# Kernel tuning notes

Measured on AMD Instinct MI355X. Metric: run time of the kernel, lower is better.

Reference implementation:

```python
import jax, jax.numpy as jnp
import numpy as np

B, N, F, H, L = 8, 512, 32, 64, 2

def setup_inputs() -> dict:
    key = jax.random.key(0)
    ks = jax.random.split(key, 16)
    s = lambda fan_in: 1.0 / np.sqrt(fan_in)
    return {
        "x": jax.random.normal(ks[0], (B, N, F), dtype=jnp.float32),
        # node encoder: Linear(F, H), stored as [in, out]
        "W_enc": jax.random.uniform(ks[1], (F, H), minval=-s(F), maxval=s(F)),
        "b_enc": jax.random.uniform(ks[2], (H,), minval=-s(F), maxval=s(F)),
        # edge MLP: Linear(2H, H) then Linear(H, 1)
        "W_e1": jax.random.uniform(ks[3], (2 * H, H), minval=-s(2 * H), maxval=s(2 * H)),
        "b_e1": jax.random.uniform(ks[4], (H,), minval=-s(2 * H), maxval=s(2 * H)),
        "W_e2": jax.random.uniform(ks[5], (H,), minval=-s(H), maxval=s(H)),
        "b_e2": jax.random.uniform(ks[6], (), minval=-s(H), maxval=s(H)),
        # per-layer message Linear(H, H)
        "W_msg": jax.random.uniform(ks[7], (L, H, H), minval=-s(H), maxval=s(H)),
        "b_msg": jax.random.uniform(ks[8], (L, H), minval=-s(H), maxval=s(H)),
        # per-layer GRUCell(H, H): gates ordered [r, z, n], stored as [in, 3H]
        "W_ih": jax.random.uniform(ks[9], (L, H, 3 * H), minval=-s(H), maxval=s(H)),
        "b_ih": jax.random.uniform(ks[10], (L, 3 * H), minval=-s(H), maxval=s(H)),
        "W_hh": jax.random.uniform(ks[11], (L, H, 3 * H), minval=-s(H), maxval=s(H)),
        "b_hh": jax.random.uniform(ks[12], (L, 3 * H), minval=-s(H), maxval=s(H)),
        # output Linear(H, 1)
        "W_out": jax.random.uniform(ks[13], (H, 1), minval=-s(H), maxval=s(H)),
        "b_out": jax.random.uniform(ks[14], (1,), minval=-s(H), maxval=s(H)),
    }

def reference(x, W_enc, b_enc, W_e1, b_e1, W_e2, b_e2, W_msg, b_msg,
              W_ih, b_ih, W_hh, b_hh, W_out, b_out):
    # Node encoding (dropout is eval-mode identity)
    h = jax.nn.relu(x @ W_enc + b_enc)  # [B, N, H]

    # Edge MLP on pairwise concat [h_i, h_j]: split W_e1 so we never build the 2H concat
    Wa, Wb = W_e1[:H], W_e1[H:]
    zi = h @ Wa                           # contribution of h_i, [B, N, H]
    zj = h @ Wb                           # contribution of h_j, [B, N, H]
    e = jax.nn.relu(zi[:, :, None, :] + zj[:, None, :, :] + b_e1)  # [B, N, N, H]
    logits = jnp.einsum('bijh,h->bij', e, W_e2) + b_e2             # [B, N, N]

    eye = jnp.eye(logits.shape[-1], dtype=bool)
    logits = jnp.where(eye[None], -jnp.inf, logits)
    adj = jax.nn.softmax(logits, axis=-1)
    adj = jnp.nan_to_num(adj, nan=0.0, posinf=0.0, neginf=0.0)

    for l in range(L):
        m = jnp.einsum('bij,bjh->bih', adj, h)             # message aggregation
        m = jax.nn.relu(m @ W_msg[l] + b_msg[l])
        # GRUCell update (gates [r, z, n])
        gi = m @ W_ih[l] + b_ih[l]
        gh = h @ W_hh[l] + b_hh[l]
        ir, iz, inn = jnp.split(gi, 3, axis=-1)
        hr, hz, hn = jnp.split(gh, 3, axis=-1)
        r = jax.nn.sigmoid(ir + hr)
        z = jax.nn.sigmoid(iz + hz)
        n = jnp.tanh(inn + r * hn)
        h = (1.0 - z) * n + z * h

    graph_emb = jnp.mean(h, axis=1)       # [B, H]
    return graph_emb @ W_out + b_out      # [B, 1]
```

## Files before the change

kernel.cpp:

```cpp
#include <hip/hip_runtime.h>
#include <math.h>

#define BB 8
#define NN 512
#define FF 32
#define HH 64
#define NEG_BIG (-1.0e30f)

__device__ __forceinline__ float lane_bcast(float v, int l) {
    return __int_as_float(__builtin_amdgcn_readlane(__float_as_int(v), l));
}

__global__ __launch_bounds__(256) void encode_kernel(
    const float* __restrict__ x, const float* __restrict__ W_enc,
    const float* __restrict__ b_enc, const float* __restrict__ W_e1,
    const float* __restrict__ b_e1,
    float* __restrict__ h, float* __restrict__ zi, float* __restrict__ zjT)
{
    const int t = threadIdx.x;
    const int hh = t & 63;
    const int qu = __builtin_amdgcn_readfirstlane(t >> 6);
    const int gR = blockIdx.x * 4 + qu;

    const float xv = x[gR * FF + (hh & 31)];
    float acc = b_enc[hh];
#pragma unroll 8
    for (int k = 0; k < FF; ++k)
        acc = fmaf(lane_bcast(xv, k), W_enc[k * HH + hh], acc);
    const float hval = fmaxf(acc, 0.f);
    h[gR * HH + hh] = hval;

    float z1 = b_e1[hh], z2 = 0.f;
#pragma unroll 8
    for (int k = 0; k < HH; ++k) {
        const float hk = lane_bcast(hval, k);
        z1 = fmaf(hk, W_e1[k * HH + hh], z1);
        z2 = fmaf(hk, W_e1[(HH + k) * HH + hh], z2);
    }
    zi[gR * HH + hh] = z1;
    zjT[((size_t)(gR >> 9) * HH + hh) * NN + (gR & (NN - 1))] = z2;
}

template <int MODE>
__global__ __launch_bounds__(512, 4) void adjlayer_kernel(
    const float* __restrict__ zi, const float* __restrict__ zjT,
    const float* __restrict__ We2, const float* __restrict__ be2,
    float* __restrict__ adjw, const float* __restrict__ h_in,
    const float* __restrict__ Wmsg, const float* __restrict__ bmsg,
    const float* __restrict__ Wih, const float* __restrict__ bih,
    const float* __restrict__ Whh, const float* __restrict__ bhh,
    float* __restrict__ h_out, float* __restrict__ partial)
{
    const int b  = blockIdx.x >> 6;
    const int i0 = (blockIdx.x & 63) << 3;
    const int t  = threadIdx.x;
    const int tj = t & 63;
    const int w  = __builtin_amdgcn_readfirstlane(t >> 6);
    const int gR0 = b * NN + i0;
    const int j   = 64 * w + tj;

    __shared__ float smem[6336];
    __shared__ float mml[8][66];
    __shared__ float hol[8][66];
    __shared__ float redm[8][8];
    __shared__ float reds[8][8];
#define RED(p, r, c)        smem[(((p) * 8) + (r)) * 66 + (c)]
#define GP(h2, k2, r, g, c) smem[(((((h2) * 2 + (k2)) * 8 + (r)) * 3 + (g)) * 66) + (c)]

    hol[w][tj] = h_in[(size_t)(gR0 + w) * HH + tj];

    float va[8];
    if (MODE == 0) {
        const float* zib = zi + (size_t)gR0 * HH;
        const float* ztb = zjT + (size_t)b * HH * NN + j;
        const float bias2 = be2[0];
        float acc[8];
#pragma unroll
        for (int r = 0; r < 8; ++r) acc[r] = bias2;

        for (int kc = 0; kc < 8; ++kc) {
            float zt[8];
#pragma unroll
            for (int kk = 0; kk < 8; ++kk)
                zt[kk] = ztb[(size_t)(kc * 8 + kk) * NN];
#pragma unroll
            for (int kk = 0; kk < 8; ++kk) {
                const int k = kc * 8 + kk;
                const float wk = We2[k];
#pragma unroll
                for (int r = 0; r < 8; ++r) {
                    const float zv = zib[r * HH + k];
                    acc[r] = fmaf(fmaxf(zv + zt[kk], 0.f), wk, acc[r]);
                }
            }
        }
#pragma unroll
        for (int r = 0; r < 8; ++r)
            if (j == i0 + r) acc[r] = NEG_BIG;

#pragma unroll
        for (int r = 0; r < 8; ++r) {
            float m = acc[r];
#pragma unroll
            for (int off = 32; off >= 1; off >>= 1) m = fmaxf(m, __shfl_xor(m, off));
            if (tj == 0) redm[w][r] = m;
        }
        __syncthreads();
        float M[8];
#pragma unroll
        for (int r = 0; r < 8; ++r) {
            float m = redm[0][r];
#pragma unroll
            for (int p = 1; p < 8; ++p) m = fmaxf(m, redm[p][r]);
            M[r] = m;
        }
#pragma unroll
        for (int r = 0; r < 8; ++r) {
            const float e = __expf(acc[r] - M[r]);
            va[r] = e;
            float s = e;
#pragma unroll
            for (int off = 32; off >= 1; off >>= 1) s += __shfl_xor(s, off);
            if (tj == 0) reds[w][r] = s;
        }
        __syncthreads();
#pragma unroll
        for (int r = 0; r < 8; ++r) {
            float s = reds[0][r];
#pragma unroll
            for (int p = 1; p < 8; ++p) s += reds[p][r];
            va[r] *= 1.0f / s;
            adjw[(size_t)(gR0 + r) * NN + j] = va[r];
        }
    } else {
#pragma unroll
        for (int r = 0; r < 8; ++r)
            va[r] = adjw[(size_t)(gR0 + r) * NN + j];
    }

    {
        const float* hq = h_in + ((size_t)b * NN + 64 * w) * HH + tj;
        float mac[8] = {0.f, 0.f, 0.f, 0.f, 0.f, 0.f, 0.f, 0.f};
#pragma unroll 4
        for (int jj = 0; jj < 64; ++jj) {
            const float hv = hq[(size_t)jj * HH];
#pragma unroll
            for (int r = 0; r < 8; ++r)
                mac[r] = fmaf(lane_bcast(va[r], jj), hv, mac[r]);
        }
#pragma unroll
        for (int r = 0; r < 8; ++r) RED(w, r, tj) = mac[r];
    }
    __syncthreads();

    {
        float m = RED(0, w, tj);
#pragma unroll
        for (int p = 1; p < 8; ++p) m += RED(p, w, tj);
        float mmv = bmsg[tj];
#pragma unroll 8
        for (int k = 0; k < HH; ++k)
            mmv = fmaf(lane_bcast(m, k), Wmsg[k * HH + tj], mmv);
        mml[w][tj] = fmaxf(mmv, 0.f);
    }
    __syncthreads();

    {
        const int half = w >> 2, kh = (w >> 1) & 1, rq = w & 1;
        const float* Wg = half ? Whh : Wih;
        const float* bg = half ? bhh : bih;
        float sreg[4];
#pragma unroll
        for (int r = 0; r < 4; ++r)
            sreg[r] = half ? hol[rq * 4 + r][tj] : mml[rq * 4 + r][tj];
        float g0[4], g1[4], g2[4];
#pragma unroll
        for (int r = 0; r < 4; ++r) {
            g0[r] = kh ? 0.f : bg[tj];
            g1[r] = kh ? 0.f : bg[64 + tj];
            g2[r] = kh ? 0.f : bg[128 + tj];
        }
        const int k0 = kh * 32;
#pragma unroll 4
        for (int kk = 0; kk < 32; ++kk) {
            const float* wk = Wg + (size_t)(k0 + kk) * 192;
            const float w0 = wk[tj], w1 = wk[64 + tj], w2 = wk[128 + tj];
#pragma unroll
            for (int r = 0; r < 4; ++r) {
                const float s = lane_bcast(sreg[r], k0 + kk);
                g0[r] = fmaf(s, w0, g0[r]);
                g1[r] = fmaf(s, w1, g1[r]);
                g2[r] = fmaf(s, w2, g2[r]);
            }
        }
#pragma unroll
        for (int r = 0; r < 4; ++r) {
            GP(half, kh, rq * 4 + r, 0, tj) = g0[r];
            GP(half, kh, rq * 4 + r, 1, tj) = g1[r];
            GP(half, kh, rq * 4 + r, 2, tj) = g2[r];
        }
    }
    __syncthreads();

    float hnew;
    {
        const float ir  = GP(0, 0, w, 0, tj) + GP(0, 1, w, 0, tj);
        const float iz  = GP(0, 0, w, 1, tj) + GP(0, 1, w, 1, tj);
        const float inn = GP(0, 0, w, 2, tj) + GP(0, 1, w, 2, tj);
        const float hr  = GP(1, 0, w, 0, tj) + GP(1, 1, w, 0, tj);
        const float hz  = GP(1, 0, w, 1, tj) + GP(1, 1, w, 1, tj);
        const float hn  = GP(1, 0, w, 2, tj) + GP(1, 1, w, 2, tj);
        const float rg = 1.f / (1.f + __expf(-(ir + hr)));
        const float zg = 1.f / (1.f + __expf(-(iz + hz)));
        const float ng = tanhf(inn + rg * hn);
        hnew = (1.f - zg) * ng + zg * hol[w][tj];
        h_out[(size_t)(gR0 + w) * HH + tj] = hnew;
    }

    if (MODE == 1) {
        __syncthreads();
        mml[w][tj] = hnew;
        __syncthreads();
        if (w == 0) {
            float s = 0.f;
#pragma unroll
            for (int r = 0; r < 8; ++r) s += mml[r][tj];
            partial[blockIdx.x * 64 + tj] = s;
        }
    }
#undef RED
#undef GP
}

__global__ __launch_bounds__(64) void readout_kernel(
    const float* __restrict__ partial, const float* __restrict__ W_out,
    const float* __restrict__ b_out, float* __restrict__ out)
{
    const int b = blockIdx.x;
    const int hh = threadIdx.x;
    float s = 0.f;
#pragma unroll 8
    for (int c = 0; c < 64; ++c)
        s += partial[(b * 64 + c) * 64 + hh];
    float v = s * (1.0f / NN) * W_out[hh];
#pragma unroll
    for (int off = 32; off >= 1; off >>= 1) v += __shfl_xor(v, off);
    if (hh == 0) out[b] = v + b_out[0];
}

extern "C" void kernel_launch(void* const* d_in, const int* in_sizes, int n_in,
                              void* d_out, int out_size, void* d_ws, size_t ws_size,
                              hipStream_t stream)
{
    const float* x     = (const float*)d_in[0];
    const float* W_enc = (const float*)d_in[1];
    const float* b_enc = (const float*)d_in[2];
    const float* W_e1  = (const float*)d_in[3];
    const float* b_e1  = (const float*)d_in[4];
    const float* W_e2  = (const float*)d_in[5];
    const float* b_e2  = (const float*)d_in[6];
    const float* W_msg = (const float*)d_in[7];
    const float* b_msg = (const float*)d_in[8];
    const float* W_ih  = (const float*)d_in[9];
    const float* b_ih  = (const float*)d_in[10];
    const float* W_hh  = (const float*)d_in[11];
    const float* b_hh  = (const float*)d_in[12];
    const float* W_out = (const float*)d_in[13];
    const float* b_out = (const float*)d_in[14];
    float* out = (float*)d_out;

    float* ws   = (float*)d_ws;
    float* h0   = ws;
    float* h1   = h0 + BB * NN * HH;
    float* zi   = h1 + BB * NN * HH;
    float* zjT  = zi + BB * NN * HH;
    float* prt  = zjT + BB * HH * NN;
    float* adjw = prt + 512 * 64;

    encode_kernel<<<BB * NN / 4, 256, 0, stream>>>(x, W_enc, b_enc, W_e1, b_e1, h0, zi, zjT);

    adjlayer_kernel<0><<<BB * (NN / 8), 512, 0, stream>>>(
        zi, zjT, W_e2, b_e2, adjw, h0,
        W_msg, b_msg, W_ih, b_ih, W_hh, b_hh, h1, nullptr);
    adjlayer_kernel<1><<<BB * (NN / 8), 512, 0, stream>>>(
        zi, zjT, W_e2, b_e2, adjw, h1,
        W_msg + HH * HH, b_msg + HH,
        W_ih + HH * 3 * HH, b_ih + 3 * HH, W_hh + HH * 3 * HH, b_hh + 3 * HH,
        h0, prt);

    readout_kernel<<<BB, 64, 0, stream>>>(prt, W_out, b_out, out);
}
```

Measured before the change: 73.25 us.

## Retile adjacency-layer kernel to 4 rows per 256-thread block with paired zj layout

Each adjlayer block now handles 4 destination rows with 4 waves instead of 8 rows with 8 waves, doubling the grid to 1024 blocks. Each thread covers two j columns. The zj projection is stored interleaved in k-pairs so it can be read as float2, and the edge-MLP accumulation keeps two partial sums per row. The GRU gate matmuls are merged into one per-wave loop, which removes the split-k smem staging and two barriers. This raises parallelism and cuts synchronisation, at the cost of reloading zj and h twice as often across blocks and a longer readout reduction.

```diff
diff --git a/kernel.cpp b/kernel.cpp
--- a/kernel.cpp
+++ b/kernel.cpp
@@ -15,7 +15,7 @@
     const float* __restrict__ x, const float* __restrict__ W_enc,
     const float* __restrict__ b_enc, const float* __restrict__ W_e1,
     const float* __restrict__ b_e1,
-    float* __restrict__ h, float* __restrict__ zi, float* __restrict__ zjT)
+    float* __restrict__ h, float* __restrict__ zi, float* __restrict__ zjT2)
 {
     const int t = threadIdx.x;
     const int hh = t & 63;
@@ -38,12 +38,13 @@
         z2 = fmaf(hk, W_e1[(HH + k) * HH + hh], z2);
     }
     zi[gR * HH + hh] = z1;
-    zjT[((size_t)(gR >> 9) * HH + hh) * NN + (gR & (NN - 1))] = z2;
+    const int b = gR >> 9, n = gR & (NN - 1);
+    zjT2[(((size_t)b * 32 + (hh >> 1)) * NN + n) * 2 + (hh & 1)] = z2;
 }
 
 template <int MODE>
-__global__ __launch_bounds__(512, 4) void adjlayer_kernel(
-    const float* __restrict__ zi, const float* __restrict__ zjT,
+__global__ __launch_bounds__(256, 4) void adjlayer_kernel(
+    const float* __restrict__ zi, const float* __restrict__ zjT2,
     const float* __restrict__ We2, const float* __restrict__ be2,
     float* __restrict__ adjw, const float* __restrict__ h_in,
     const float* __restrict__ Wmsg, const float* __restrict__ bmsg,
@@ -51,185 +52,151 @@
     const float* __restrict__ Whh, const float* __restrict__ bhh,
     float* __restrict__ h_out, float* __restrict__ partial)
 {
-    const int b  = blockIdx.x >> 6;
-    const int i0 = (blockIdx.x & 63) << 3;
+    const int b  = blockIdx.x >> 7;
+    const int i0 = (blockIdx.x & 127) << 2;
     const int t  = threadIdx.x;
     const int tj = t & 63;
     const int w  = __builtin_amdgcn_readfirstlane(t >> 6);
     const int gR0 = b * NN + i0;
-    const int j   = 64 * w + tj;
-
-    __shared__ float smem[6336];
-    __shared__ float mml[8][66];
-    __shared__ float hol[8][66];
-    __shared__ float redm[8][8];
-    __shared__ float reds[8][8];
-#define RED(p, r, c)        smem[(((p) * 8) + (r)) * 66 + (c)]
-#define GP(h2, k2, r, g, c) smem[(((((h2) * 2 + (k2)) * 8 + (r)) * 3 + (g)) * 66) + (c)]
-
-    hol[w][tj] = h_in[(size_t)(gR0 + w) * HH + tj];
-
-    float va[8];
+
+    __shared__ float RED[4][4][66];
+    __shared__ float redm[4][4], reds[4][4];
+    __shared__ float hsum[4][66];
+
+    const float hreg = h_in[(size_t)(gR0 + w) * HH + tj];
+
+    float va[4][2];
     if (MODE == 0) {
-        const float* zib = zi + (size_t)gR0 * HH;
-        const float* ztb = zjT + (size_t)b * HH * NN + j;
+        const float2* zi2 = (const float2*)(zi + (size_t)gR0 * HH);
+        const float2* we2 = (const float2*)We2;
+        const float2* zt2 = (const float2*)zjT2 + (size_t)b * 32 * NN;
+        const int j0 = 128 * w + tj, j1 = j0 + 64;
+
+        float2 a2[4][2];
+#pragma unroll
+        for (int r = 0; r < 4; ++r) {
+            a2[r][0] = make_float2(0.f, 0.f);
+            a2[r][1] = make_float2(0.f, 0.f);
+        }
+#pragma unroll 8
+        for (int k2 = 0; k2 < 32; ++k2) {
+            const float2 z0 = zt2[(size_t)k2 * NN + j0];
+            const float2 z1 = zt2[(size_t)k2 * NN + j1];
+            const float2 wk = we2[k2];
+#pragma unroll
+            for (int r = 0; r < 4; ++r) {
+                const float2 zv = zi2[r * 32 + k2];
+                a2[r][0].x = fmaf(fmaxf(zv.x + z0.x, 0.f), wk.x, a2[r][0].x);
+                a2[r][0].y = fmaf(fmaxf(zv.y + z0.y, 0.f), wk.y, a2[r][0].y);
+                a2[r][1].x = fmaf(fmaxf(zv.x + z1.x, 0.f), wk.x, a2[r][1].x);
+                a2[r][1].y = fmaf(fmaxf(zv.y + z1.y, 0.f), wk.y, a2[r][1].y);
+            }
+        }
         const float bias2 = be2[0];
-        float acc[8];
-#pragma unroll
-        for (int r = 0; r < 8; ++r) acc[r] = bias2;
-
-        for (int kc = 0; kc < 8; ++kc) {
-            float zt[8];
-#pragma unroll
-            for (int kk = 0; kk < 8; ++kk)
-                zt[kk] = ztb[(size_t)(kc * 8 + kk) * NN];
-#pragma unroll
-            for (int kk = 0; kk < 8; ++kk) {
-                const int k = kc * 8 + kk;
-                const float wk = We2[k];
-#pragma unroll
-                for (int r = 0; r < 8; ++r) {
-                    const float zv = zib[r * HH + k];
-                    acc[r] = fmaf(fmaxf(zv + zt[kk], 0.f), wk, acc[r]);
-                }
-            }
-        }
-#pragma unroll
-        for (int r = 0; r < 8; ++r)
-            if (j == i0 + r) acc[r] = NEG_BIG;
-
-#pragma unroll
-        for (int r = 0; r < 8; ++r) {
-            float m = acc[r];
-#pragma unroll
-            for (int off = 32; off >= 1; off >>= 1) m = fmaxf(m, __shfl_xor(m, off));
+        float acc[4][2];
+#pragma unroll
+        for (int r = 0; r < 4; ++r) {
+            acc[r][0] = a2[r][0].x + a2[r][0].y + bias2;
+            acc[r][1] = a2[r][1].x + a2[r][1].y + bias2;
+            if (j0 == i0 + r) acc[r][0] = NEG_BIG;
+            if (j1 == i0 + r) acc[r][1] = NEG_BIG;
+        }
+
+#pragma unroll
+        for (int r = 0; r < 4; ++r) {
+            float m = fmaxf(acc[r][0], acc[r][1]);
+#pragma unroll
+            for (int off = 32; off >= 1; off >>= 1)
+                m = fmaxf(m, __shfl_xor(m, off));
             if (tj == 0) redm[w][r] = m;
         }
         __syncthreads();
-        float M[8];
-#pragma unroll
-        for (int r = 0; r < 8; ++r) {
-            float m = redm[0][r];
-#pragma unroll
-            for (int p = 1; p < 8; ++p) m = fmaxf(m, redm[p][r]);
-            M[r] = m;
-        }
-#pragma unroll
-        for (int r = 0; r < 8; ++r) {
-            const float e = __expf(acc[r] - M[r]);
-            va[r] = e;
-            float s = e;
+        float M[4];
+#pragma unroll
+        for (int r = 0; r < 4; ++r)
+            M[r] = fmaxf(fmaxf(redm[0][r], redm[1][r]),
+                         fmaxf(redm[2][r], redm[3][r]));
+#pragma unroll
+        for (int r = 0; r < 4; ++r) {
+            va[r][0] = __expf(acc[r][0] - M[r]);
+            va[r][1] = __expf(acc[r][1] - M[r]);
+            float s = va[r][0] + va[r][1];
 #pragma unroll
             for (int off = 32; off >= 1; off >>= 1) s += __shfl_xor(s, off);
             if (tj == 0) reds[w][r] = s;
         }
         __syncthreads();
 #pragma unroll
-        for (int r = 0; r < 8; ++r) {
-            float s = reds[0][r];
-#pragma unroll
-            for (int p = 1; p < 8; ++p) s += reds[p][r];
-            va[r] *= 1.0f / s;
-            adjw[(size_t)(gR0 + r) * NN + j] = va[r];
+        for (int r = 0; r < 4; ++r) {
+            const float inv = 1.0f /
+                (reds[0][r] + reds[1][r] + reds[2][r] + reds[3][r]);
+            va[r][0] *= inv; va[r][1] *= inv;
+            adjw[(size_t)(gR0 + r) * NN + j0] = va[r][0];
+            adjw[(size_t)(gR0 + r) * NN + j1] = va[r][1];
         }
     } else {
-#pragma unroll
-        for (int r = 0; r < 8; ++r)
-            va[r] = adjw[(size_t)(gR0 + r) * NN + j];
+        const int j0 = 128 * w + tj;
+#pragma unroll
+        for (int r = 0; r < 4; ++r) {
+            va[r][0] = adjw[(size_t)(gR0 + r) * NN + j0];
+            va[r][1] = adjw[(size_t)(gR0 + r) * NN + j0 + 64];
+        }
     }
 
     {
-        const float* hq = h_in + ((size_t)b * NN + 64 * w) * HH + tj;
-        float mac[8] = {0.f, 0.f, 0.f, 0.f, 0.f, 0.f, 0.f, 0.f};
+        const float* hq = h_in + ((size_t)b * NN + 128 * w) * HH + tj;
+        float mac[4] = {0.f, 0.f, 0.f, 0.f};
 #pragma unroll 4
         for (int jj = 0; jj < 64; ++jj) {
-            const float hv = hq[(size_t)jj * HH];
-#pragma unroll
-            for (int r = 0; r < 8; ++r)
-                mac[r] = fmaf(lane_bcast(va[r], jj), hv, mac[r]);
-        }
-#pragma unroll
-        for (int r = 0; r < 8; ++r) RED(w, r, tj) = mac[r];
+            const float hv0 = hq[(size_t)jj * HH];
+            const float hv1 = hq[(size_t)(jj + 64) * HH];
+#pragma unroll
+            for (int r = 0; r < 4; ++r) {
+                mac[r] = fmaf(lane_bcast(va[r][0], jj), hv0, mac[r]);
+                mac[r] = fmaf(lane_bcast(va[r][1], jj), hv1, mac[r]);
+            }
+        }
+#pragma unroll
+        for (int r = 0; r < 4; ++r) RED[w][r][tj] = mac[r];
     }
     __syncthreads();
 
-    {
-        float m = RED(0, w, tj);
-#pragma unroll
-        for (int p = 1; p < 8; ++p) m += RED(p, w, tj);
-        float mmv = bmsg[tj];
-#pragma unroll 8
-        for (int k = 0; k < HH; ++k)
-            mmv = fmaf(lane_bcast(m, k), Wmsg[k * HH + tj], mmv);
-        mml[w][tj] = fmaxf(mmv, 0.f);
-    }
-    __syncthreads();
-
-    {
-        const int half = w >> 2, kh = (w >> 1) & 1, rq = w & 1;
-        const float* Wg = half ? Whh : Wih;
-        const float* bg = half ? bhh : bih;
-        float sreg[4];
-#pragma unroll
-        for (int r = 0; r < 4; ++r)
-            sreg[r] = half ? hol[rq * 4 + r][tj] : mml[rq * 4 + r][tj];
-        float g0[4], g1[4], g2[4];
-#pragma unroll
-        for (int r = 0; r < 4; ++r) {
-            g0[r] = kh ? 0.f : bg[tj];
-            g1[r] = kh ? 0.f : bg[64 + tj];
-            g2[r] = kh ? 0.f : bg[128 + tj];
-        }
-        const int k0 = kh * 32;
+    const float m = RED[0][w][tj] + RED[1][w][tj] + RED[2][w][tj] + RED[3][w][tj];
+    float mmv = bmsg[tj];
+#pragma unroll 8
+    for (int k = 0; k < HH; ++k)
+        mmv = fmaf(lane_bcast(m, k), Wmsg[k * HH + tj], mmv);
+    mmv = fmaxf(mmv, 0.f);
+
+    float g0 = bih[tj], g1 = bih[64 + tj], g2 = bih[128 + tj];
+    float g3 = bhh[tj], g4 = bhh[64 + tj], g5 = bhh[128 + tj];
 #pragma unroll 4
-        for (int kk = 0; kk < 32; ++kk) {
-            const float* wk = Wg + (size_t)(k0 + kk) * 192;
-            const float w0 = wk[tj], w1 = wk[64 + tj], w2 = wk[128 + tj];
-#pragma unroll
-            for (int r = 0; r < 4; ++r) {
-                const float s = lane_bcast(sreg[r], k0 + kk);
-                g0[r] = fmaf(s, w0, g0[r]);
-                g1[r] = fmaf(s, w1, g1[r]);
-                g2[r] = fmaf(s, w2, g2[r]);
-            }
-        }
-#pragma unroll
-        for (int r = 0; r < 4; ++r) {
-            GP(half, kh, rq * 4 + r, 0, tj) = g0[r];
-            GP(half, kh, rq * 4 + r, 1, tj) = g1[r];
-            GP(half, kh, rq * 4 + r, 2, tj) = g2[r];
-        }
-    }
-    __syncthreads();
-
-    float hnew;
-    {
-        const float ir  = GP(0, 0, w, 0, tj) + GP(0, 1, w, 0, tj);
-        const float iz  = GP(0, 0, w, 1, tj) + GP(0, 1, w, 1, tj);
-        const float inn = GP(0, 0, w, 2, tj) + GP(0, 1, w, 2, tj);
-        const float hr  = GP(1, 0, w, 0, tj) + GP(1, 1, w, 0, tj);
-        const float hz  = GP(1, 0, w, 1, tj) + GP(1, 1, w, 1, tj);
-        const float hn  = GP(1, 0, w, 2, tj) + GP(1, 1, w, 2, tj);
-        const float rg = 1.f / (1.f + __expf(-(ir + hr)));
-        const float zg = 1.f / (1.f + __expf(-(iz + hz)));
-        const float ng = tanhf(inn + rg * hn);
-        hnew = (1.f - zg) * ng + zg * hol[w][tj];
-        h_out[(size_t)(gR0 + w) * HH + tj] = hnew;
-    }
+    for (int k = 0; k < HH; ++k) {
+        const float smm = lane_bcast(mmv, k);
+        const float sh  = lane_bcast(hreg, k);
+        const float* wi = Wih + (size_t)k * 192;
+        const float* wh = Whh + (size_t)k * 192;
+        g0 = fmaf(smm, wi[tj], g0);
+        g1 = fmaf(smm, wi[64 + tj], g1);
+        g2 = fmaf(smm, wi[128 + tj], g2);
+        g3 = fmaf(sh, wh[tj], g3);
+        g4 = fmaf(sh, wh[64 + tj], g4);
+        g5 = fmaf(sh, wh[128 + tj], g5);
+    }
+    const float rg = 1.f / (1.f + __expf(-(g0 + g3)));
+    const float zg = 1.f / (1.f + __expf(-(g1 + g4)));
+    const float ng = tanhf(g2 + rg * g5);
+    const float hnew = (1.f - zg) * ng + zg * hreg;
+    h_out[(size_t)(gR0 + w) * HH + tj] = hnew;
 
     if (MODE == 1) {
-        __syncthreads();
-        mml[w][tj] = hnew;
+        hsum[w][tj] = hnew;
         __syncthreads();
         if (w == 0) {
-            float s = 0.f;
-#pragma unroll
-            for (int r = 0; r < 8; ++r) s += mml[r][tj];
-            partial[blockIdx.x * 64 + tj] = s;
-        }
-    }
-#undef RED
-#undef GP
+            partial[blockIdx.x * 64 + tj] =
+                hsum[0][tj] + hsum[1][tj] + hsum[2][tj] + hsum[3][tj];
+        }
+    }
 }
 
 __global__ __launch_bounds__(64) void readout_kernel(
@@ -240,8 +207,8 @@
     const int hh = threadIdx.x;
     float s = 0.f;
 #pragma unroll 8
-    for (int c = 0; c < 64; ++c)
-        s += partial[(b * 64 + c) * 64 + hh];
+    for (int c = 0; c < 128; ++c)
+        s += partial[(b * 128 + c) * 64 + hh];
     float v = s * (1.0f / NN) * W_out[hh];
 #pragma unroll
     for (int off = 32; off >= 1; off >>= 1) v += __shfl_xor(v, off);
@@ -273,17 +240,18 @@
     float* h0   = ws;
     float* h1   = h0 + BB * NN * HH;
     float* zi   = h1 + BB * NN * HH;
-    float* zjT  = zi + BB * NN * HH;
-    float* prt  = zjT + BB * HH * NN;
-    float* adjw = prt + 512 * 64;
-
-    encode_kernel<<<BB * NN / 4, 256, 0, stream>>>(x, W_enc, b_enc, W_e1, b_e1, h0, zi, zjT);
-
-    adjlayer_kernel<0><<<BB * (NN / 8), 512, 0, stream>>>(
-        zi, zjT, W_e2, b_e2, adjw, h0,
+    float* zjT2 = zi + BB * NN * HH;
+    float* prt  = zjT2 + BB * NN * HH;
+    float* adjw = prt + 1024 * 64;
+
+    encode_kernel<<<BB * NN / 4, 256, 0, stream>>>(
+        x, W_enc, b_enc, W_e1, b_e1, h0, zi, zjT2);
+
+    adjlayer_kernel<0><<<BB * (NN / 4), 256, 0, stream>>>(
+        zi, zjT2, W_e2, b_e2, adjw, h0,
         W_msg, b_msg, W_ih, b_ih, W_hh, b_hh, h1, nullptr);
-    adjlayer_kernel<1><<<BB * (NN / 8), 512, 0, stream>>>(
-        zi, zjT, W_e2, b_e2, adjw, h1,
+    adjlayer_kernel<1><<<BB * (NN / 4), 256, 0, stream>>>(
+        zi, zjT2, W_e2, b_e2, adjw, h1,
         W_msg + HH * HH, b_msg + HH,
         W_ih + HH * 3 * HH, b_ih + 3 * HH, W_hh + HH * 3 * HH, b_hh + 3 * HH,
         h0, prt);
```

New measurement: 82.33 us. +12.4%, slower.
